# Performance work log

Hardware: AMD Instinct MI355X
Metric: run time of the kernel (lower is better)

The kernel has to match this reference:

```python
import jax, jax.numpy as jnp
import numpy as np

B, S, D = 2, 2048, 1024
H, DK, DV = 16, 64, 64
DF = 4096
EPS = 1e-5


def _layer_norm(x, g, b):
    mu = jnp.mean(x, axis=-1, keepdims=True)
    var = jnp.mean((x - mu) ** 2, axis=-1, keepdims=True)
    return (x - mu) * jax.lax.rsqrt(var + EPS) * g + b


def setup_inputs() -> dict:
    key = jax.random.key(0)
    ks = jax.random.split(key, 12)
    s = lambda fan_in: 1.0 / np.sqrt(fan_in)
    return {
        "enc_input": jax.random.normal(ks[0], (B, S, D), dtype=jnp.float32),
        "wq": jax.random.uniform(ks[1], (D, H * DK), jnp.float32, -s(D), s(D)),
        "wk": jax.random.uniform(ks[2], (D, H * DK), jnp.float32, -s(D), s(D)),
        "wv": jax.random.uniform(ks[3], (D, H * DV), jnp.float32, -s(D), s(D)),
        "wo": jax.random.uniform(ks[4], (H * DV, D), jnp.float32, -s(H * DV), s(H * DV)),
        "w1": jax.random.uniform(ks[5], (D, DF), jnp.float32, -s(D), s(D)),
        "b1": jax.random.uniform(ks[6], (DF,), jnp.float32, -s(D), s(D)),
        "w2": jax.random.uniform(ks[7], (DF, D), jnp.float32, -s(DF), s(DF)),
        "b2": jax.random.uniform(ks[8], (D,), jnp.float32, -s(DF), s(DF)),
        "ln1_g": jnp.ones((D,), jnp.float32),
        "ln1_b": jnp.zeros((D,), jnp.float32),
        "ln2_g": jnp.ones((D,), jnp.float32),
        "ln2_b": jnp.zeros((D,), jnp.float32),
    }


def reference(enc_input, wq, wk, wv, wo, w1, b1, w2, b2, ln1_g, ln1_b, ln2_g, ln2_b):
    x = enc_input
    # QKV projections -> [B, H, S, d]
    q = (x @ wq).reshape(B, S, H, DK).transpose(0, 2, 1, 3)
    k = (x @ wk).reshape(B, S, H, DK).transpose(0, 2, 1, 3)
    v = (x @ wv).reshape(B, S, H, DV).transpose(0, 2, 1, 3)
    # scaled dot-product attention (scale = 1/sqrt(d_k), dropout is identity at eval)
    score = jnp.einsum("bhqd,bhkd->bhqk", q, k) / jnp.sqrt(jnp.float32(DK))
    attn = jax.nn.softmax(score, axis=-1)
    ctx = jnp.einsum("bhqk,bhkd->bhqd", attn, v)
    ctx = ctx.transpose(0, 2, 1, 3).reshape(B, S, H * DV)
    atn_out = ctx @ wo
    # Add & Norm 1
    h = _layer_norm(x + atn_out, ln1_g, ln1_b)
    # FFN
    ffn = jax.nn.relu(h @ w1 + b1) @ w2 + b2
    # Add & Norm 2
    return _layer_norm(h + ffn, ln2_g, ln2_b)
```

## Files before the change

### kernel.cpp

```cpp
#include <hip/hip_runtime.h>
#include <hip/hip_bf16.h>

typedef __bf16 bf16;
typedef __bf16 bf16x4 __attribute__((ext_vector_type(4)));
typedef __bf16 bf16x8 __attribute__((ext_vector_type(8)));
typedef float  f32x4  __attribute__((ext_vector_type(4)));

#define KB 2
#define KS 2048
#define KD 1024
#define KH 16
#define KM (KB*KS)
#define KQKVN 3072
#define KDF 4096

__device__ __forceinline__ f32x4 mfma16(bf16x8 a, bf16x8 b, f32x4 c) {
  return __builtin_amdgcn_mfma_f32_16x16x32_bf16(a, b, c, 0, 0, 0);
}

__device__ __forceinline__ float exp2_hw(float x) {
  float r;
  asm("v_exp_f32 %0, %1" : "=v"(r) : "v"(x));
  return r;
}

__device__ __forceinline__ void g2l16(const bf16* g, bf16* l) {
  __builtin_amdgcn_global_load_lds(
      (const __attribute__((address_space(1))) unsigned int*)g,
      (__attribute__((address_space(3))) unsigned int*)l, 16, 0, 0);
}

__global__ __launch_bounds__(256) void cvt_bf16_kernel(const float* __restrict__ in,
                                                       bf16* __restrict__ out, int n) {
  int i = (blockIdx.x * 256 + threadIdx.x) * 4;
  if (i >= n) return;
  f32x4 v = *reinterpret_cast<const f32x4*>(in + i);
  bf16x4 o;
  o[0] = (bf16)v[0]; o[1] = (bf16)v[1]; o[2] = (bf16)v[2]; o[3] = (bf16)v[3];
  *reinterpret_cast<bf16x4*>(out + i) = o;
}

struct WT4 { const float* src[4]; bf16* dst[4]; };

__global__ __launch_bounds__(256) void wtrans4_kernel(WT4 jobs) {
  __shared__ float tile[32][33];
  const float* W = jobs.src[blockIdx.z];
  bf16* WT = jobs.dst[blockIdx.z];
  const int n0 = blockIdx.x * 32, k0 = blockIdx.y * 32;
  const int tx = threadIdx.x & 31, ty = threadIdx.x >> 5;
#pragma unroll
  for (int j = ty; j < 32; j += 8) tile[j][tx] = W[(size_t)(k0 + j) * 1024 + n0 + tx];
  __syncthreads();
#pragma unroll
  for (int j = ty; j < 32; j += 8)
    WT[(size_t)(n0 + j) * 1024 + k0 + tx] = (bf16)tile[tx][j];
}

__global__ __launch_bounds__(256) void wtrans_big_kernel(const float* __restrict__ w1,
                                                         bf16* __restrict__ w1T,
                                                         const float* __restrict__ w2,
                                                         bf16* __restrict__ w2T) {
  __shared__ float tile[32][33];
  const float* W; bf16* WT; int K, N, n0, k0;
  if (blockIdx.z == 0) {
    W = w1; WT = w1T; K = 1024; N = 4096;
    n0 = blockIdx.x * 32; k0 = blockIdx.y * 32;
  } else {
    W = w2; WT = w2T; K = 4096; N = 1024;
    n0 = blockIdx.y * 32; k0 = blockIdx.x * 32;
  }
  const int tx = threadIdx.x & 31, ty = threadIdx.x >> 5;
#pragma unroll
  for (int j = ty; j < 32; j += 8) tile[j][tx] = W[(size_t)(k0 + j) * N + n0 + tx];
  __syncthreads();
#pragma unroll
  for (int j = ty; j < 32; j += 8) WT[(size_t)(n0 + j) * K + k0 + tx] = (bf16)tile[tx][j];
}

struct P4 { bf16* p[4]; };

template <typename OUT_T, bool RELU, bool HAS_BIAS, bool SPLITK, bool QKVPACK>
__global__ __launch_bounds__(512, 2) void gemm8p(const bf16* __restrict__ A,
                                                 const bf16* __restrict__ BT,
                                                 OUT_T* __restrict__ C, P4 pr,
                                                 const float* __restrict__ bias,
                                                 int M, int N, int K, int Kslice) {
  extern __shared__ __align__(16) bf16 sm[];
  const int tid = threadIdx.x, lane = tid & 63, w = tid >> 6;
  const int wr = w >> 2, wc = w & 3;
  const int gx = gridDim.x;
  const int nwg = gx * gridDim.y;
  int flat = blockIdx.y * gx + blockIdx.x;
  flat = (flat & 7) * (nwg >> 3) + (flat >> 3);
  const int bn = (flat % gx) * 256;
  const int bm = (flat / gx) * 256;
  const int z = blockIdx.z;
  const int NT = (SPLITK ? Kslice : K) >> 6;
  const int lr = lane & 15, hi = lane >> 4;
  const int sqrow = tid >> 3;
  const int sslot = tid & 7;
  const bf16* Abase = A + (size_t)bm * K + (SPLITK ? z * Kslice : 0);
  const bf16* Bbase = BT + (size_t)bn * K + (SPLITK ? z * Kslice : 0);
  auto stageQ = [&](int t, int p) {
    const int row = p * 64 + sqrow;
    const int col = (sslot ^ (row & 7)) * 8;
    bf16* dst = sm + (size_t)(t & 1) * 32768 + p * 4096 + w * 512;
    g2l16(Abase + (size_t)row * K + t * 64 + col, dst);
    g2l16(Bbase + (size_t)row * K + t * 64 + col, dst + 16384);
  };
  f32x4 acc[8][4] = {};
  stageQ(0, 0); stageQ(0, 1); stageQ(0, 2); stageQ(0, 3);
  for (int t = 0; t < NT; t++) {
    const char* sa = (const char*)(sm + (size_t)(t & 1) * 32768);
    const char* sb = sa + 32768;
    if (t + 1 < NT) {
      stageQ(t + 1, 0);
      stageQ(t + 1, 1);
      asm volatile("s_waitcnt vmcnt(4)" ::: "memory");
    } else {
      asm volatile("s_waitcnt vmcnt(0)" ::: "memory");
    }
    __builtin_amdgcn_sched_barrier(0);
    __builtin_amdgcn_s_barrier();
    __builtin_amdgcn_sched_barrier(0);
    if (t + 1 < NT) { stageQ(t + 1, 2); stageQ(t + 1, 3); }
    bf16x8 af[4], bfr[4];
#pragma unroll
    for (int mfp = 0; mfp < 4; mfp++) {
      const int row = wr * 128 + mfp * 16 + lr;
      af[mfp] = *(const bf16x8*)(sa + row * 128 + ((hi ^ (row & 7)) * 16));
    }
#pragma unroll
    for (int nf = 0; nf < 4; nf++) {
      const int row = wc * 64 + nf * 16 + lr;
      bfr[nf] = *(const bf16x8*)(sb + row * 128 + ((hi ^ (row & 7)) * 16));
    }
    __builtin_amdgcn_s_setprio(1);
#pragma unroll
    for (int mfp = 0; mfp < 4; mfp++)
#pragma unroll
      for (int nf = 0; nf < 4; nf++)
        acc[mfp][nf] = mfma16(af[mfp], bfr[nf], acc[mfp][nf]);
    __builtin_amdgcn_s_setprio(0);
#pragma unroll
    for (int mfp = 0; mfp < 4; mfp++) {
      const int row = wr * 128 + 64 + mfp * 16 + lr;
      af[mfp] = *(const bf16x8*)(sa + row * 128 + ((hi ^ (row & 7)) * 16));
    }
    __builtin_amdgcn_s_setprio(1);
#pragma unroll
    for (int mfp = 0; mfp < 4; mfp++)
#pragma unroll
      for (int nf = 0; nf < 4; nf++)
        acc[4 + mfp][nf] = mfma16(af[mfp], bfr[nf], acc[4 + mfp][nf]);
    __builtin_amdgcn_s_setprio(0);
#pragma unroll
    for (int mfp = 0; mfp < 4; mfp++) {
      const int row = wr * 128 + mfp * 16 + lr;
      af[mfp] = *(const bf16x8*)(sa + row * 128 + (((4 + hi) ^ (row & 7)) * 16));
    }
#pragma unroll
    for (int nf = 0; nf < 4; nf++) {
      const int row = wc * 64 + nf * 16 + lr;
      bfr[nf] = *(const bf16x8*)(sb + row * 128 + (((4 + hi) ^ (row & 7)) * 16));
    }
    __builtin_amdgcn_s_setprio(1);
#pragma unroll
    for (int mfp = 0; mfp < 4; mfp++)
#pragma unroll
      for (int nf = 0; nf < 4; nf++)
        acc[mfp][nf] = mfma16(af[mfp], bfr[nf], acc[mfp][nf]);
    __builtin_amdgcn_s_setprio(0);
#pragma unroll
    for (int mfp = 0; mfp < 4; mfp++) {
      const int row = wr * 128 + 64 + mfp * 16 + lr;
      af[mfp] = *(const bf16x8*)(sa + row * 128 + (((4 + hi) ^ (row & 7)) * 16));
    }
    __builtin_amdgcn_s_setprio(1);
#pragma unroll
    for (int mfp = 0; mfp < 4; mfp++)
#pragma unroll
      for (int nf = 0; nf < 4; nf++)
        acc[4 + mfp][nf] = mfma16(af[mfp], bfr[nf], acc[4 + mfp][nf]);
    __builtin_amdgcn_s_setprio(0);
    __builtin_amdgcn_sched_barrier(0);
    __builtin_amdgcn_s_barrier();
    __builtin_amdgcn_sched_barrier(0);
  }
  const int rg = hi * 4, cl = lr;
  if (QKVPACK && (bn >> 10) == 1) {
    bf16* kp_ = pr.p[0];
    const int b_ = bm >> 11;
    const int sb_ = (bm & 2047) + wr * 128;
#pragma unroll
    for (int mf = 0; mf < 8; mf++)
#pragma unroll
      for (int nf = 0; nf < 4; nf++) {
        const int col_loc = (bn & 1023) + wc * 64 + nf * 16 + cl;
        const int hh = col_loc >> 6, dd = col_loc & 63;
        bf16* base = kp_ + (size_t)(b_ * 16 + hh) * (KS * 64) + dd;
#pragma unroll
        for (int i = 0; i < 4; i++)
          base[(size_t)(sb_ + mf * 16 + rg + i) * 64] = (bf16)acc[mf][nf][i];
      }
  } else if (QKVPACK && (bn >> 10) == 2) {
    bf16* vt_ = pr.p[1];
    const int b_ = bm >> 11;
    const int sb_ = (bm & 2047) + wr * 128;
    const int pib = ((hi & 2) << 3) | ((hi & 1) << 3);
#pragma unroll
    for (int mf = 0; mf < 8; mf++) {
      const int s_hi = sb_ + (mf >> 2) * 64;
      const int pibase = pib | ((mf & 2) << 4) | ((mf & 1) << 2);
#pragma unroll
      for (int nf = 0; nf < 4; nf++) {
        const int col_loc = (bn & 1023) + wc * 64 + nf * 16 + cl;
        const int hh = col_loc >> 6, dd = col_loc & 63;
        bf16x4 o;
#pragma unroll
        for (int i = 0; i < 4; i++) o[i] = (bf16)acc[mf][nf][i];
        *(bf16x4*)(vt_ + (size_t)(b_ * 16 + hh) * (64 * KS) +
                   (size_t)dd * KS + s_hi + pibase) = o;
      }
    }
  } else if (SPLITK) {
    bf16* P = pr.p[z];
#pragma unroll
    for (int mf = 0; mf < 8; mf++)
#pragma unroll
      for (int nf = 0; nf < 4; nf++) {
        const int col = bn + wc * 64 + nf * 16 + cl;
#pragma unroll
        for (int i = 0; i < 4; i++) {
          const int row = bm + wr * 128 + mf * 16 + rg + i;
          P[(size_t)row * N + col] = (bf16)acc[mf][nf][i];
        }
      }
  } else {
#pragma unroll
    for (int mf = 0; mf < 8; mf++)
#pragma unroll
      for (int nf = 0; nf < 4; nf++) {
        const int col = bn + wc * 64 + nf * 16 + cl;
        float bv = 0.f;
        if (HAS_BIAS) bv = bias[col];
#pragma unroll
        for (int i = 0; i < 4; i++) {
          const int row = bm + wr * 128 + mf * 16 + rg + i;
          float v = acc[mf][nf][i] + bv;
          if (RELU) v = fmaxf(v, 0.f);
          C[(size_t)row * N + col] = (OUT_T)v;
        }
      }
  }
}

template <typename OUT_T, bool RELU, bool HAS_BIAS, int BN>
__global__ __launch_bounds__(256) void gemm_bt(const bf16* __restrict__ A,
                                               const bf16* __restrict__ BT,
                                               OUT_T* __restrict__ C,
                                               const float* __restrict__ bias,
                                               int M, int N, int K) {
  constexpr int NF = BN / 32;
  __shared__ __align__(16) bf16 sa[2][128 * 32];
  __shared__ __align__(16) bf16 sb[2][BN * 32];
  const int t = threadIdx.x, lane = t & 63, w = t >> 6;
  const int gx = gridDim.x;
  const int nwg = gx * gridDim.y;
  int flat = blockIdx.y * gx + blockIdx.x;
  if ((nwg & 7) == 0) flat = (flat & 7) * (nwg >> 3) + (flat >> 3);
  const int bn = (flat % gx) * BN;
  const int bm = (flat / gx) * 128;
  const int wr = w >> 1, wc = w & 1;
  const int wcol = wc * (BN / 2);
  const int lr = lane & 15, lk = (lane >> 4) * 8;
  const int srow = w * 16 + (lane >> 2);
  const int scol = (lane & 3) * 8;
  f32x4 acc[4][NF] = {};
  const int NT = K >> 5;
  auto stage = [&](int kt, int buf) {
#pragma unroll
    for (int i = 0; i < 2; i++)
      g2l16(A + (size_t)(bm + i * 64 + srow) * K + kt * 32 + scol,
            &sa[buf][(i * 64 + w * 16) * 32]);
#pragma unroll
    for (int i = 0; i < BN / 64; i++)
      g2l16(BT + (size_t)(bn + i * 64 + srow) * K + kt * 32 + scol,
            &sb[buf][(i * 64 + w * 16) * 32]);
  };
  stage(0, 0);
  int cur = 0;
  for (int kt = 0; kt < NT; kt++) {
    __syncthreads();
    if (kt + 1 < NT) stage(kt + 1, cur ^ 1);
    bf16x8 af[4], bfr[NF];
#pragma unroll
    for (int m = 0; m < 4; m++)
      af[m] = *(const bf16x8*)&sa[cur][(wr * 64 + m * 16 + lr) * 32 + lk];
#pragma unroll
    for (int n = 0; n < NF; n++)
      bfr[n] = *(const bf16x8*)&sb[cur][(wcol + n * 16 + lr) * 32 + lk];
#pragma unroll
    for (int m = 0; m < 4; m++)
#pragma unroll
      for (int n = 0; n < NF; n++)
        acc[m][n] = mfma16(af[m], bfr[n], acc[m][n]);
    cur ^= 1;
  }
  const int rg = (lane >> 4) * 4, cl = lane & 15;
#pragma unroll
  for (int m = 0; m < 4; m++)
#pragma unroll
    for (int n = 0; n < NF; n++) {
      const int col = bn + wcol + n * 16 + cl;
      float bv = 0.f;
      if (HAS_BIAS) bv = bias[col];
#pragma unroll
      for (int i = 0; i < 4; i++) {
        const int row = bm + wr * 64 + m * 16 + rg + i;
        float v = acc[m][n][i] + bv;
        if (RELU) v = fmaxf(v, 0.f);
        C[(size_t)row * N + col] = (OUT_T)v;
      }
    }
}

__global__ __launch_bounds__(256) void attn_kernel(const bf16* __restrict__ qkv,
                                                   const bf16* __restrict__ kp,
                                                   const bf16* __restrict__ vt,
                                                   bf16* __restrict__ ctx) {
  __shared__ __align__(16) bf16 ksm[4][64 * 64];
  __shared__ __align__(16) bf16 vsm[4][64 * 64];
  const int t = threadIdx.x, lane = t & 63, w = t >> 6;
  const int flat = blockIdx.y * 16 + blockIdx.x;
  const int xcd = flat & 7, jj = flat >> 3;
  const int bh = xcd + 8 * (jj >> 4);
  const int qb = jj & 15;
  const int b = bh >> 4, h = bh & 15;
  const int qbase = qb * 128 + w * 32;
  const int lr = lane & 15, hi = lane >> 4;
  const int lk = hi * 8, rg = hi * 4, cl = lr;

  bf16x8 aq[2][2];
#pragma unroll
  for (int m = 0; m < 2; m++)
#pragma unroll
    for (int kk = 0; kk < 2; kk++) {
      bf16x8 v = *reinterpret_cast<const bf16x8*>(
          &qkv[(size_t)(b * KS + qbase + m * 16 + lr) * KQKVN + h * 64 + kk * 32 + lk]);
#pragma unroll
      for (int e = 0; e < 8; e++) v[e] = (bf16)((float)v[e] * 0.18033688f);
      aq[m][kk] = v;
    }
  bf16x8 ones;
#pragma unroll
  for (int j = 0; j < 8; j++) ones[j] = (bf16)1.0f;

  const bf16* kpb = kp + (size_t)bh * KS * 64;
  const bf16* vtb = vt + (size_t)bh * 64 * KS;

  auto stageKV = [&](int tt) {
    const int kt0 = tt * 64;
    bf16* kd = &ksm[tt & 3][0];
    bf16* vd = &vsm[tt & 3][0];
#pragma unroll
    for (int i = 0; i < 2; i++) {
      const int q = i * 4096 + w * 1024 + (lane << 4);
      const int row = q >> 7;
      const int slot = ((q >> 4) & 7) ^ (row & 7);
      g2l16(kpb + (size_t)(kt0 + row) * 64 + slot * 8, kd + ((i * 4096 + w * 1024) >> 1));
      g2l16(vtb + (size_t)row * KS + kt0 + slot * 8,   vd + ((i * 4096 + w * 1024) >> 1));
    }
  };

  f32x4 accd[2][4] = {};
  f32x4 lsumv[2] = {};
  f32x4 sc[2][4];
#pragma unroll
  for (int m = 0; m < 2; m++)
#pragma unroll
    for (int n = 0; n < 4; n++)
#pragma unroll
      for (int e = 0; e < 4; e++) sc[m][n][e] = 0.f;

  stageKV(0); stageKV(1); stageKV(2);
  asm volatile("s_waitcnt vmcnt(8)" ::: "memory");
  __builtin_amdgcn_sched_barrier(0);
  __builtin_amdgcn_s_barrier();
  __builtin_amdgcn_sched_barrier(0);
  {
    const char* kb = (const char*)&ksm[0][0];
    bf16x8 bk[4][2];
#pragma unroll
    for (int n = 0; n < 4; n++)
#pragma unroll
      for (int kk = 0; kk < 2; kk++) {
        const int row = n * 16 + lr;
        bk[n][kk] = *(const bf16x8*)(kb + row * 128 +
                                     ((kk * 64 + hi * 16) ^ ((row & 7) << 4)));
      }
    __builtin_amdgcn_s_setprio(1);
#pragma unroll
    for (int m = 0; m < 2; m++)
#pragma unroll
      for (int n = 0; n < 4; n++)
#pragma unroll
        for (int kk = 0; kk < 2; kk++)
          sc[m][n] = mfma16(bk[n][kk], aq[m][kk], sc[m][n]);
    __builtin_amdgcn_s_setprio(0);
  }
  const int NT = KS / 64;
  for (int tt = 0; tt < NT; tt++) {
    if (tt + 1 < NT) {
      if (tt + 2 < NT) asm volatile("s_waitcnt vmcnt(4)" ::: "memory");
      else             asm volatile("s_waitcnt vmcnt(0)" ::: "memory");
      __builtin_amdgcn_sched_barrier(0);
      __builtin_amdgcn_s_barrier();
      __builtin_amdgcn_sched_barrier(0);
      if (tt + 3 < NT) stageKV(tt + 3);
    }
    bf16x8 pa[2][2];
#pragma unroll
    for (int m = 0; m < 2; m++) {
      float p[4][4];
#pragma unroll
      for (int n = 0; n < 4; n++)
#pragma unroll
        for (int i = 0; i < 4; i++)
          p[n][i] = exp2_hw(sc[m][n][i]);
#pragma unroll
      for (int kk = 0; kk < 2; kk++) {
        bf16x8 v;
#pragma unroll
        for (int j = 0; j < 8; j++) v[j] = (bf16)p[kk * 2 + (j >> 2)][j & 3];
        pa[m][kk] = v;
      }
    }
    if (tt + 1 < NT) {
      const char* kb = (const char*)&ksm[(tt + 1) & 3][0];
      bf16x8 bk[4][2];
#pragma unroll
      for (int n = 0; n < 4; n++)
#pragma unroll
        for (int kk = 0; kk < 2; kk++) {
          const int row = n * 16 + lr;
          bk[n][kk] = *(const bf16x8*)(kb + row * 128 +
                                       ((kk * 64 + hi * 16) ^ ((row & 7) << 4)));
        }
      f32x4 scn[2][4];
#pragma unroll
      for (int m = 0; m < 2; m++)
#pragma unroll
        for (int n = 0; n < 4; n++) {
#pragma unroll
          for (int e = 0; e < 4; e++) scn[m][n][e] = 0.f;
#pragma unroll
          for (int kk = 0; kk < 2; kk++)
            scn[m][n] = mfma16(bk[n][kk], aq[m][kk], scn[m][n]);
        }
#pragma unroll
      for (int m = 0; m < 2; m++)
#pragma unroll
        for (int n = 0; n < 4; n++) sc[m][n] = scn[m][n];
    }
    const char* vb = (const char*)&vsm[tt & 3][0];
    bf16x8 bv[4][2];
#pragma unroll
    for (int dt = 0; dt < 4; dt++)
#pragma unroll
      for (int kk = 0; kk < 2; kk++) {
        const int row = dt * 16 + lr;
        bv[dt][kk] = *(const bf16x8*)(vb + row * 128 +
                                      ((kk * 64 + hi * 16) ^ ((row & 7) << 4)));
      }
    __builtin_amdgcn_s_setprio(1);
#pragma unroll
    for (int m = 0; m < 2; m++) {
#pragma unroll
      for (int dt = 0; dt < 4; dt++)
#pragma unroll
        for (int kk = 0; kk < 2; kk++)
          accd[m][dt] = mfma16(pa[m][kk], bv[dt][kk], accd[m][dt]);
      lsumv[m] = mfma16(pa[m][0], ones, lsumv[m]);
      lsumv[m] = mfma16(pa[m][1], ones, lsumv[m]);
    }
    __builtin_amdgcn_s_setprio(0);
  }
#pragma unroll
  for (int m = 0; m < 2; m++)
#pragma unroll
    for (int dt = 0; dt < 4; dt++)
#pragma unroll
      for (int i = 0; i < 4; i++)
        ctx[(size_t)(b * KS + qbase + m * 16 + rg + i) * KD + h * 64 + dt * 16 + cl] =
            (bf16)(accd[m][dt][i] / lsumv[m][i]);
}

template <bool ABF, bool BBF, bool OBF>
__global__ __launch_bounds__(256) void ln_kernel(const void* __restrict__ aptr,
                                                 const void* __restrict__ bptr,
                                                 const float* __restrict__ g,
                                                 const float* __restrict__ bet,
                                                 void* __restrict__ outp) {
  const int row = blockIdx.x;
  const int t = threadIdx.x;
  const int lane = t & 63, wid = t >> 6;
  float v[4];
  {
    float a[4], bb[4];
    if (ABF) {
      bf16x4 av = *reinterpret_cast<const bf16x4*>(
          (const bf16*)aptr + (size_t)row * KD + t * 4);
#pragma unroll
      for (int j = 0; j < 4; j++) a[j] = (float)av[j];
    } else {
      f32x4 av = *reinterpret_cast<const f32x4*>(
          (const float*)aptr + (size_t)row * KD + t * 4);
#pragma unroll
      for (int j = 0; j < 4; j++) a[j] = av[j];
    }
    if (BBF) {
      bf16x4 bv = *reinterpret_cast<const bf16x4*>(
          (const bf16*)bptr + (size_t)row * KD + t * 4);
#pragma unroll
      for (int j = 0; j < 4; j++) bb[j] = (float)bv[j];
    } else {
      f32x4 bv = *reinterpret_cast<const f32x4*>(
          (const float*)bptr + (size_t)row * KD + t * 4);
#pragma unroll
      for (int j = 0; j < 4; j++) bb[j] = bv[j];
    }
#pragma unroll
    for (int j = 0; j < 4; j++) v[j] = a[j] + bb[j];
  }
  float s = 0.f, s2 = 0.f;
#pragma unroll
  for (int j = 0; j < 4; j++) { s += v[j]; s2 += v[j] * v[j]; }
#pragma unroll
  for (int off = 32; off; off >>= 1) {
    s += __shfl_xor(s, off, 64);
    s2 += __shfl_xor(s2, off, 64);
  }
  __shared__ float red[8];
  if (lane == 0) { red[wid] = s; red[wid + 4] = s2; }
  __syncthreads();
  s = red[0] + red[1] + red[2] + red[3];
  s2 = red[4] + red[5] + red[6] + red[7];
  const float mu = s * (1.f / KD);
  const float var = s2 * (1.f / KD) - mu * mu;
  const float rs = rsqrtf(var + 1e-5f);
  if (OBF) {
    bf16x4 o;
#pragma unroll
    for (int j = 0; j < 4; j++)
      o[j] = (bf16)((v[j] - mu) * rs * g[t * 4 + j] + bet[t * 4 + j]);
    *reinterpret_cast<bf16x4*>((bf16*)outp + (size_t)row * KD + t * 4) = o;
  } else {
    f32x4 o;
#pragma unroll
    for (int j = 0; j < 4; j++)
      o[j] = (v[j] - mu) * rs * g[t * 4 + j] + bet[t * 4 + j];
    *reinterpret_cast<f32x4*>((float*)outp + (size_t)row * KD + t * 4) = o;
  }
}

__global__ __launch_bounds__(256) void ln2_fused_kernel(const bf16* __restrict__ hh,
                                                        const bf16* __restrict__ p0,
                                                        const bf16* __restrict__ p1,
                                                        const bf16* __restrict__ p2,
                                                        const bf16* __restrict__ p3,
                                                        const float* __restrict__ b2,
                                                        const float* __restrict__ g,
                                                        const float* __restrict__ bet,
                                                        float* __restrict__ outp) {
  const int row = blockIdx.x;
  const int t = threadIdx.x;
  const int lane = t & 63, wid = t >> 6;
  const size_t base = (size_t)row * KD + t * 4;
  bf16x4 hv = *(const bf16x4*)(hh + base);
  bf16x4 a0 = *(const bf16x4*)(p0 + base);
  bf16x4 a1 = *(const bf16x4*)(p1 + base);
  bf16x4 a2 = *(const bf16x4*)(p2 + base);
  bf16x4 a3 = *(const bf16x4*)(p3 + base);
  f32x4 bv = *(const f32x4*)(b2 + t * 4);
  float v[4];
#pragma unroll
  for (int j = 0; j < 4; j++)
    v[j] = (float)hv[j] + (float)a0[j] + (float)a1[j] + (float)a2[j] + (float)a3[j] + bv[j];
  float s = 0.f, s2 = 0.f;
#pragma unroll
  for (int j = 0; j < 4; j++) { s += v[j]; s2 += v[j] * v[j]; }
#pragma unroll
  for (int off = 32; off; off >>= 1) {
    s += __shfl_xor(s, off, 64);
    s2 += __shfl_xor(s2, off, 64);
  }
  __shared__ float red[8];
  if (lane == 0) { red[wid] = s; red[wid + 4] = s2; }
  __syncthreads();
  s = red[0] + red[1] + red[2] + red[3];
  s2 = red[4] + red[5] + red[6] + red[7];
  const float mu = s * (1.f / KD);
  const float var = s2 * (1.f / KD) - mu * mu;
  const float rs = rsqrtf(var + 1e-5f);
  f32x4 o;
#pragma unroll
  for (int j = 0; j < 4; j++)
    o[j] = (v[j] - mu) * rs * g[t * 4 + j] + bet[t * 4 + j];
  *reinterpret_cast<f32x4*>(outp + base) = o;
}

extern "C" void kernel_launch(void* const* d_in, const int* in_sizes, int n_in,
                              void* d_out, int out_size, void* d_ws, size_t ws_size,
                              hipStream_t stream) {
  const float* x     = (const float*)d_in[0];
  const float* wq    = (const float*)d_in[1];
  const float* wk    = (const float*)d_in[2];
  const float* wv    = (const float*)d_in[3];
  const float* wo    = (const float*)d_in[4];
  const float* w1    = (const float*)d_in[5];
  const float* b1    = (const float*)d_in[6];
  const float* w2    = (const float*)d_in[7];
  const float* b2    = (const float*)d_in[8];
  const float* ln1g  = (const float*)d_in[9];
  const float* ln1b  = (const float*)d_in[10];
  const float* ln2g  = (const float*)d_in[11];
  const float* ln2b  = (const float*)d_in[12];
  float* out = (float*)d_out;

  char* ws = (char*)d_ws;
  bf16*  x_bf   = (bf16*)(ws + 0);
  bf16*  wqkvT  = (bf16*)(ws + 8388608);
  bf16*  woT    = (bf16*)(ws + 14680064);
  bf16*  w1T    = (bf16*)(ws + 16777216);
  bf16*  w2T    = (bf16*)(ws + 25165824);
  bf16*  qkv    = (bf16*)(ws + 33554432);
  bf16*  kp     = (bf16*)(ws + 58720256);
  bf16*  vt     = (bf16*)(ws + 67108864);
  bf16*  ctx    = (bf16*)(ws + 75497472);
  bf16*  proj_bf= (bf16*)(ws + 83886080);
  bf16*  h_bf   = (bf16*)(ws + 8388608);
  bf16*  ffn1   = qkv;
  P4 pk;
  pk.p[0] = kp; pk.p[1] = vt; pk.p[2] = nullptr; pk.p[3] = nullptr;
  P4 pr;
  pr.p[0] = (bf16*)(ws + 0);
  pr.p[1] = (bf16*)(ws + 16777216);
  pr.p[2] = (bf16*)(ws + 67108864);
  pr.p[3] = (bf16*)(ws + 75497472);
  P4 pzero = {};

  cvt_bf16_kernel<<<dim3(KM * KD / 1024), 256, 0, stream>>>(x, x_bf, KM * KD);
  WT4 jobs;
  jobs.src[0] = wq; jobs.src[1] = wk; jobs.src[2] = wv; jobs.src[3] = wo;
  jobs.dst[0] = wqkvT;
  jobs.dst[1] = wqkvT + 1024 * 1024;
  jobs.dst[2] = wqkvT + 2048 * 1024;
  jobs.dst[3] = woT;
  wtrans4_kernel<<<dim3(32, 32, 4), 256, 0, stream>>>(jobs);
  wtrans_big_kernel<<<dim3(128, 32, 2), 256, 0, stream>>>(w1, w1T, w2, w2T);

  gemm8p<bf16, false, false, false, true>
      <<<dim3(KQKVN / 256, KM / 256, 1), 512, 131072, stream>>>(
      x_bf, wqkvT, qkv, pk, nullptr, KM, KQKVN, KD, KD);

  attn_kernel<<<dim3(KS / 128, KB * KH), 256, 0, stream>>>(qkv, kp, vt, ctx);

  gemm_bt<bf16, false, false, 64><<<dim3(KD / 64, KM / 128), 256, 0, stream>>>(
      ctx, woT, proj_bf, nullptr, KM, KD, KD);

  ln_kernel<true, true, true><<<dim3(KM), 256, 0, stream>>>(
      x_bf, proj_bf, ln1g, ln1b, h_bf);

  gemm8p<bf16, true, true, false, false>
      <<<dim3(KDF / 256, KM / 256, 1), 512, 131072, stream>>>(
      h_bf, w1T, ffn1, pzero, b1, KM, KDF, KD, KD);

  gemm8p<bf16, false, false, true, false>
      <<<dim3(KD / 256, KM / 256, 4), 512, 131072, stream>>>(
      ffn1, w2T, (bf16*)nullptr, pr, nullptr, KM, KD, KDF, KDF / 4);

  ln2_fused_kernel<<<dim3(KM), 256, 0, stream>>>(
      h_bf, pr.p[0], pr.p[1], pr.p[2], pr.p[3], b2, ln2g, ln2b, out);
}
```

Baseline: 214.7 us.

## Shrink attention query tile to 64 rows and simplify KV pipeline to double buffering

The attention kernel now handles 16 query rows per wave (64 per block) instead of 32, which doubles the grid, and the XCD-aware block mapping is updated to match. The 4-deep KV ring with QK^T software-pipelined one tile ahead is replaced by a 2-buffer scheme that computes scores within the same iteration and uses a second barrier before refilling. This lowers register and LDS use so more blocks fit per CU and more blocks run in parallel. The cost is that each K/V tile is loaded twice as often and MFMA latency has less overlap inside a wave.

```diff
diff --git a/kernel.cpp b/kernel.cpp
--- a/kernel.cpp
+++ b/kernel.cpp
@@ -329,29 +329,27 @@
                                                    const bf16* __restrict__ kp,
                                                    const bf16* __restrict__ vt,
                                                    bf16* __restrict__ ctx) {
-  __shared__ __align__(16) bf16 ksm[4][64 * 64];
-  __shared__ __align__(16) bf16 vsm[4][64 * 64];
+  __shared__ __align__(16) bf16 ksm[2][64 * 64];
+  __shared__ __align__(16) bf16 vsm[2][64 * 64];
   const int t = threadIdx.x, lane = t & 63, w = t >> 6;
-  const int flat = blockIdx.y * 16 + blockIdx.x;
+  const int flat = blockIdx.y * 32 + blockIdx.x;
   const int xcd = flat & 7, jj = flat >> 3;
-  const int bh = xcd + 8 * (jj >> 4);
-  const int qb = jj & 15;
+  const int bh = xcd + 8 * (jj >> 5);
+  const int qb = jj & 31;
   const int b = bh >> 4, h = bh & 15;
-  const int qbase = qb * 128 + w * 32;
+  const int qbase = qb * 64 + w * 16;
   const int lr = lane & 15, hi = lane >> 4;
   const int lk = hi * 8, rg = hi * 4, cl = lr;
 
-  bf16x8 aq[2][2];
-#pragma unroll
-  for (int m = 0; m < 2; m++)
-#pragma unroll
-    for (int kk = 0; kk < 2; kk++) {
-      bf16x8 v = *reinterpret_cast<const bf16x8*>(
-          &qkv[(size_t)(b * KS + qbase + m * 16 + lr) * KQKVN + h * 64 + kk * 32 + lk]);
-#pragma unroll
-      for (int e = 0; e < 8; e++) v[e] = (bf16)((float)v[e] * 0.18033688f);
-      aq[m][kk] = v;
-    }
+  bf16x8 aq[2];
+#pragma unroll
+  for (int kk = 0; kk < 2; kk++) {
+    bf16x8 v = *reinterpret_cast<const bf16x8*>(
+        &qkv[(size_t)(b * KS + qbase + lr) * KQKVN + h * 64 + kk * 32 + lk]);
+#pragma unroll
+    for (int e = 0; e < 8; e++) v[e] = (bf16)((float)v[e] * 0.18033688f);
+    aq[kk] = v;
+  }
   bf16x8 ones;
 #pragma unroll
   for (int j = 0; j < 8; j++) ones[j] = (bf16)1.0f;
@@ -361,8 +359,8 @@
 
   auto stageKV = [&](int tt) {
     const int kt0 = tt * 64;
-    bf16* kd = &ksm[tt & 3][0];
-    bf16* vd = &vsm[tt & 3][0];
+    bf16* kd = &ksm[tt & 1][0];
+    bf16* vd = &vsm[tt & 1][0];
 #pragma unroll
     for (int i = 0; i < 2; i++) {
       const int q = i * 4096 + w * 1024 + (lane << 4);
@@ -373,23 +371,19 @@
     }
   };
 
-  f32x4 accd[2][4] = {};
-  f32x4 lsumv[2] = {};
-  f32x4 sc[2][4];
-#pragma unroll
-  for (int m = 0; m < 2; m++)
-#pragma unroll
-    for (int n = 0; n < 4; n++)
-#pragma unroll
-      for (int e = 0; e < 4; e++) sc[m][n][e] = 0.f;
-
-  stageKV(0); stageKV(1); stageKV(2);
-  asm volatile("s_waitcnt vmcnt(8)" ::: "memory");
-  __builtin_amdgcn_sched_barrier(0);
-  __builtin_amdgcn_s_barrier();
-  __builtin_amdgcn_sched_barrier(0);
-  {
-    const char* kb = (const char*)&ksm[0][0];
+  f32x4 accd[4] = {};
+  f32x4 lsumv = {};
+
+  stageKV(0); stageKV(1);
+  const int NT = KS / 64;
+  for (int tt = 0; tt < NT; tt++) {
+    if (tt + 1 < NT) asm volatile("s_waitcnt vmcnt(4)" ::: "memory");
+    else             asm volatile("s_waitcnt vmcnt(0)" ::: "memory");
+    __builtin_amdgcn_sched_barrier(0);
+    __builtin_amdgcn_s_barrier();
+    __builtin_amdgcn_sched_barrier(0);
+    const char* kb = (const char*)&ksm[tt & 1][0];
+    const char* vb = (const char*)&vsm[tt & 1][0];
     bf16x8 bk[4][2];
 #pragma unroll
     for (int n = 0; n < 4; n++)
@@ -399,71 +393,30 @@
         bk[n][kk] = *(const bf16x8*)(kb + row * 128 +
                                      ((kk * 64 + hi * 16) ^ ((row & 7) << 4)));
       }
+    f32x4 sc[4] = {};
     __builtin_amdgcn_s_setprio(1);
 #pragma unroll
-    for (int m = 0; m < 2; m++)
+    for (int n = 0; n < 4; n++)
+#pragma unroll
+      for (int kk = 0; kk < 2; kk++)
+        sc[n] = mfma16(bk[n][kk], aq[kk], sc[n]);
+    __builtin_amdgcn_s_setprio(0);
+    bf16x8 pa[2];
+    {
+      float p[4][4];
 #pragma unroll
       for (int n = 0; n < 4; n++)
 #pragma unroll
-        for (int kk = 0; kk < 2; kk++)
-          sc[m][n] = mfma16(bk[n][kk], aq[m][kk], sc[m][n]);
-    __builtin_amdgcn_s_setprio(0);
-  }
-  const int NT = KS / 64;
-  for (int tt = 0; tt < NT; tt++) {
-    if (tt + 1 < NT) {
-      if (tt + 2 < NT) asm volatile("s_waitcnt vmcnt(4)" ::: "memory");
-      else             asm volatile("s_waitcnt vmcnt(0)" ::: "memory");
-      __builtin_amdgcn_sched_barrier(0);
-      __builtin_amdgcn_s_barrier();
-      __builtin_amdgcn_sched_barrier(0);
-      if (tt + 3 < NT) stageKV(tt + 3);
-    }
-    bf16x8 pa[2][2];
-#pragma unroll
-    for (int m = 0; m < 2; m++) {
-      float p[4][4];
-#pragma unroll
-      for (int n = 0; n < 4; n++)
-#pragma unroll
         for (int i = 0; i < 4; i++)
-          p[n][i] = exp2_hw(sc[m][n][i]);
+          p[n][i] = exp2_hw(sc[n][i]);
 #pragma unroll
       for (int kk = 0; kk < 2; kk++) {
         bf16x8 v;
 #pragma unroll
         for (int j = 0; j < 8; j++) v[j] = (bf16)p[kk * 2 + (j >> 2)][j & 3];
-        pa[m][kk] = v;
-      }
-    }
-    if (tt + 1 < NT) {
-      const char* kb = (const char*)&ksm[(tt + 1) & 3][0];
-      bf16x8 bk[4][2];
-#pragma unroll
-      for (int n = 0; n < 4; n++)
-#pragma unroll
-        for (int kk = 0; kk < 2; kk++) {
-          const int row = n * 16 + lr;
-          bk[n][kk] = *(const bf16x8*)(kb + row * 128 +
-                                       ((kk * 64 + hi * 16) ^ ((row & 7) << 4)));
-        }
-      f32x4 scn[2][4];
-#pragma unroll
-      for (int m = 0; m < 2; m++)
-#pragma unroll
-        for (int n = 0; n < 4; n++) {
-#pragma unroll
-          for (int e = 0; e < 4; e++) scn[m][n][e] = 0.f;
-#pragma unroll
-          for (int kk = 0; kk < 2; kk++)
-            scn[m][n] = mfma16(bk[n][kk], aq[m][kk], scn[m][n]);
-        }
-#pragma unroll
-      for (int m = 0; m < 2; m++)
-#pragma unroll
-        for (int n = 0; n < 4; n++) sc[m][n] = scn[m][n];
-    }
-    const char* vb = (const char*)&vsm[tt & 3][0];
+        pa[kk] = v;
+      }
+    }
     bf16x8 bv[4][2];
 #pragma unroll
     for (int dt = 0; dt < 4; dt++)
@@ -475,25 +428,24 @@
       }
     __builtin_amdgcn_s_setprio(1);
 #pragma unroll
-    for (int m = 0; m < 2; m++) {
-#pragma unroll
-      for (int dt = 0; dt < 4; dt++)
-#pragma unroll
-        for (int kk = 0; kk < 2; kk++)
-          accd[m][dt] = mfma16(pa[m][kk], bv[dt][kk], accd[m][dt]);
-      lsumv[m] = mfma16(pa[m][0], ones, lsumv[m]);
-      lsumv[m] = mfma16(pa[m][1], ones, lsumv[m]);
-    }
+    for (int dt = 0; dt < 4; dt++)
+#pragma unroll
+      for (int kk = 0; kk < 2; kk++)
+        accd[dt] = mfma16(pa[kk], bv[dt][kk], accd[dt]);
+    lsumv = mfma16(pa[0], ones, lsumv);
+    lsumv = mfma16(pa[1], ones, lsumv);
     __builtin_amdgcn_s_setprio(0);
-  }
-#pragma unroll
-  for (int m = 0; m < 2; m++)
-#pragma unroll
-    for (int dt = 0; dt < 4; dt++)
-#pragma unroll
-      for (int i = 0; i < 4; i++)
-        ctx[(size_t)(b * KS + qbase + m * 16 + rg + i) * KD + h * 64 + dt * 16 + cl] =
-            (bf16)(accd[m][dt][i] / lsumv[m][i]);
+    __builtin_amdgcn_sched_barrier(0);
+    __builtin_amdgcn_s_barrier();
+    __builtin_amdgcn_sched_barrier(0);
+    if (tt + 2 < NT) stageKV(tt + 2);
+  }
+#pragma unroll
+  for (int dt = 0; dt < 4; dt++)
+#pragma unroll
+    for (int i = 0; i < 4; i++)
+      ctx[(size_t)(b * KS + qbase + rg + i) * KD + h * 64 + dt * 16 + cl] =
+          (bf16)(accd[dt][i] / lsumv[i]);
 }
 
 template <bool ABF, bool BBF, bool OBF>
@@ -664,7 +616,7 @@
       <<<dim3(KQKVN / 256, KM / 256, 1), 512, 131072, stream>>>(
       x_bf, wqkvT, qkv, pk, nullptr, KM, KQKVN, KD, KD);
 
-  attn_kernel<<<dim3(KS / 128, KB * KH), 256, 0, stream>>>(qkv, kp, vt, ctx);
+  attn_kernel<<<dim3(KS / 64, KB * KH), 256, 0, stream>>>(qkv, kp, vt, ctx);
 
   gemm_bt<bf16, false, false, 64><<<dim3(KD / 64, KM / 128), 256, 0, stream>>>(
       ctx, woT, proj_bf, nullptr, KM, KD, KD);
```

After: 221.6 us. +3.2%, slower.
